# Optimization experiments

Hardware: AMD Instinct MI355X
Metric: run time of the kernel (lower is better)

The kernel has to match this reference:

```python
import jax, jax.numpy as jnp
import numpy as np

VOCAB, EMB, HID, CTXD = 32000, 512, 1024, 2048
B, T, L = 64, 64, 64

def setup_inputs() -> dict:
    key = jax.random.key(0)
    ks = jax.random.split(key, 10)
    return {
        "tgt": jax.random.randint(ks[0], (B, T), 0, VOCAB, dtype=jnp.int64 if jax.config.jax_enable_x64 else jnp.int32),
        "ctx": jax.random.normal(ks[1], (B, L, CTXD), dtype=jnp.float32),
        "h0": jax.random.normal(ks[2], (B, HID), dtype=jnp.float32),
        "ctx_lengths": jax.random.randint(ks[3], (B,), 1, L + 1),
        "emb_table": jax.random.normal(ks[4], (VOCAB, EMB), dtype=jnp.float32) * 0.01,
        "W_a": jax.random.normal(ks[5], (HID, CTXD), dtype=jnp.float32) * 0.01,
        "W_ih": jax.random.normal(ks[6], (3 * HID, EMB + CTXD), dtype=jnp.float32) * 0.01,
        "W_hh": jax.random.normal(ks[7], (3 * HID, HID), dtype=jnp.float32) * 0.01,
        "b_ih": jnp.zeros((3 * HID,), dtype=jnp.float32),
        "b_hh": jnp.zeros((3 * HID,), dtype=jnp.float32),
    }

def reference(tgt, ctx, h0, ctx_lengths, emb_table, W_a, W_ih, W_hh, b_ih, b_hh):
    H = h0.shape[-1]
    Lc = ctx.shape[1]
    # length mask over context positions: [B, L]
    mask = jnp.arange(Lc)[None, :] < ctx_lengths[:, None]
    # precompute 'general' attention projection of ctx: [B, L, H]
    ctxW = jnp.einsum('blc,hc->blh', ctx, W_a)
    emb = emb_table[tgt]  # [B, T, E]

    def step(h, e_t):
        # Bahdanau-style: attend with previous hidden state
        scores = jnp.einsum('bh,blh->bl', h, ctxW)
        scores = jnp.where(mask, scores, jnp.float32(-1e9))
        attn = jax.nn.softmax(scores, axis=-1)
        c_t = jnp.einsum('bl,blc->bc', attn, ctx)  # [B, CTXD]
        x = jnp.concatenate([e_t, c_t], axis=-1)   # [B, E+CTXD]
        gx = x @ W_ih.T + b_ih                      # [B, 3H]
        gh = h @ W_hh.T + b_hh                      # [B, 3H]
        r = jax.nn.sigmoid(gx[:, :H] + gh[:, :H])
        z = jax.nn.sigmoid(gx[:, H:2 * H] + gh[:, H:2 * H])
        n = jnp.tanh(gx[:, 2 * H:] + r * gh[:, 2 * H:])
        h_new = (1.0 - z) * n + z * h
        return h_new, h_new

    h_last, outs = jax.lax.scan(step, h0, jnp.swapaxes(emb, 0, 1))
    return jnp.swapaxes(outs, 0, 1), h_last  # (B, T, H), (B, H)
```

## Files before the change

kernel.cpp:

```cpp
#include <hip/hip_runtime.h>
#include <hip/hip_bf16.h>


using short8 = __attribute__((ext_vector_type(8))) short;
using f32x4  = __attribute__((ext_vector_type(4))) float;

#define FLAG_ACC 1
#define FLAG_BF  2

__device__ __forceinline__ void gld16(const void* g, void* l) {
  __builtin_amdgcn_global_load_lds(
      (const __attribute__((address_space(1))) unsigned int*)g,
      (__attribute__((address_space(3))) unsigned int*)l, 16, 0, 0);
}


__global__ __launch_bounds__(256) void split_bf16_kernel(
    const float* __restrict__ x, __hip_bfloat16* __restrict__ hi,
    __hip_bfloat16* __restrict__ lo, int n)
{
  int i = blockIdx.x * blockDim.x + threadIdx.x;
  int stride = gridDim.x * blockDim.x;
  for (; i < n; i += stride) {
    float v = x[i];
    __hip_bfloat16 h = __float2bfloat16(v);
    hi[i] = h;
    lo[i] = __float2bfloat16(v - __bfloat162float(h));
  }
}

__global__ __launch_bounds__(256) void prep_weights(
    const float* __restrict__ Wih, const float* __restrict__ Whh,
    const float* __restrict__ bih, const float* __restrict__ bhh,
    __hip_bfloat16* __restrict__ WcH, __hip_bfloat16* __restrict__ WcL,
    __hip_bfloat16* __restrict__ We,
    __hip_bfloat16* __restrict__ WhH, __hip_bfloat16* __restrict__ WhL,
    float* __restrict__ bihp, float* __restrict__ bhhp)
{
  const int jp = blockIdx.x;
  const int u = jp / 3, g = jp - 3 * u;
  const int src = g * 1024 + u;
  for (int c = threadIdx.x; c < 2048; c += 256) {
    float v = Wih[(size_t)src * 2560 + 512 + c];
    __hip_bfloat16 h = __float2bfloat16(v);
    WcH[(size_t)jp * 2048 + c] = h;
    WcL[(size_t)jp * 2048 + c] = __float2bfloat16(v - __bfloat162float(h));
  }
  for (int c = threadIdx.x; c < 512; c += 256)
    We[(size_t)jp * 512 + c] = __float2bfloat16(Wih[(size_t)src * 2560 + c]);
  for (int c = threadIdx.x; c < 1024; c += 256) {
    float v = Whh[(size_t)src * 1024 + c];
    __hip_bfloat16 h = __float2bfloat16(v);
    WhH[(size_t)jp * 1024 + c] = h;
    WhL[(size_t)jp * 1024 + c] = __float2bfloat16(v - __bfloat162float(h));
  }
  if (threadIdx.x == 0) { bihp[jp] = bih[src]; bhhp[jp] = bhh[src]; }
}

__global__ __launch_bounds__(256) void emb_gather(
    const int* __restrict__ tgt, const float* __restrict__ table,
    __hip_bfloat16* __restrict__ outb)
{
  const int row = blockIdx.x;
  const int v = tgt[row];
  for (int c = threadIdx.x; c < 512; c += 256)
    outb[(size_t)row * 512 + c] = __float2bfloat16(table[(size_t)v * 512 + c]);
}

__global__ __launch_bounds__(256) void h0_init(
    const float* __restrict__ h0, float* __restrict__ hf,
    __hip_bfloat16* __restrict__ hhi, __hip_bfloat16* __restrict__ hlo)
{
  const int i = blockIdx.x * 256 + threadIdx.x;
  float v = h0[i];
  hf[i] = v;
  __hip_bfloat16 h = __float2bfloat16(v);
  hhi[i] = h;
  hlo[i] = __float2bfloat16(v - __bfloat162float(h));
}


__global__ __launch_bounds__(256) void gemm_bt(
    const short* __restrict__ A, const short* __restrict__ B,
    float* __restrict__ Cf, __hip_bfloat16* __restrict__ Cb,
    const float* __restrict__ bias, int M, int N, int K, int flags)
{
  __shared__ __align__(16) short As[128 * 32];
  __shared__ __align__(16) short Bs[128 * 32];
  const int tid = threadIdx.x, lane = tid & 63, w = tid >> 6;
  const int m0 = blockIdx.y * 128, n0 = blockIdx.x * 128;
  const int wm = (w >> 1) * 64, wn = (w & 1) * 64;
  const int srow = lane >> 2;
  const int scol = (((lane & 3) ^ ((lane >> 3) & 3)) * 8);
  f32x4 zero = {0.f, 0.f, 0.f, 0.f};
  f32x4 acc[4][4];
#pragma unroll
  for (int i = 0; i < 4; ++i)
#pragma unroll
    for (int j = 0; j < 4; ++j) acc[i][j] = zero;

  for (int k0 = 0; k0 < K; k0 += 32) {
    __syncthreads();
#pragma unroll
    for (int s = 0; s < 2; ++s) {
      const int chunk = w * 2 + s;
      const int r = chunk * 16 + srow;
      gld16(A + (size_t)(m0 + r) * K + k0 + scol, As + chunk * 512);
      gld16(B + (size_t)(n0 + r) * K + k0 + scol, Bs + chunk * 512);
    }
    __syncthreads();
    const int fm = lane & 15, fq = lane >> 4;
    const int cbs = (fq ^ ((fm >> 1) & 3)) * 8;
    short8 af[4], bq[4];
#pragma unroll
    for (int i = 0; i < 4; ++i)
      af[i] = *(const short8*)(As + (wm + i * 16 + fm) * 32 + cbs);
#pragma unroll
    for (int j = 0; j < 4; ++j)
      bq[j] = *(const short8*)(Bs + (wn + j * 16 + fm) * 32 + cbs);
#pragma unroll
    for (int i = 0; i < 4; ++i)
#pragma unroll
      for (int j = 0; j < 4; ++j)
        acc[i][j] = __builtin_amdgcn_mfma_f32_16x16x32_bf16(af[i], bq[j], acc[i][j], 0, 0, 0);
  }

  const int cn = lane & 15, cq = (lane >> 4) * 4;
#pragma unroll
  for (int i = 0; i < 4; ++i)
#pragma unroll
    for (int j = 0; j < 4; ++j)
#pragma unroll
      for (int r = 0; r < 4; ++r) {
        const int m = m0 + wm + i * 16 + cq + r;
        const int n = n0 + wn + j * 16 + cn;
        float v = acc[i][j][r];
        if (flags & FLAG_ACC) v += Cf[(size_t)m * N + n];
        if (bias) v += bias[n];
        if (flags & FLAG_BF) Cb[(size_t)m * N + n] = __float2bfloat16(v);
        else                 Cf[(size_t)m * N + n] = v;
      }
}


__global__ __launch_bounds__(256) void gemm_bt3(
    const short* __restrict__ AH, const short* __restrict__ AL,
    const short* __restrict__ BH, const short* __restrict__ BL,
    float* __restrict__ Cf, int M, int N, int K)
{
  __shared__ __align__(16) short AsH[128 * 32];
  __shared__ __align__(16) short AsL[128 * 32];
  __shared__ __align__(16) short BsH[128 * 32];
  __shared__ __align__(16) short BsL[128 * 32];
  const int tid = threadIdx.x, lane = tid & 63, w = tid >> 6;
  const int m0 = blockIdx.y * 128, n0 = blockIdx.x * 128;
  const int wm = (w >> 1) * 64, wn = (w & 1) * 64;
  const int srow = lane >> 2;
  const int scol = (((lane & 3) ^ ((lane >> 3) & 3)) * 8);
  f32x4 zero = {0.f, 0.f, 0.f, 0.f};
  f32x4 acc[4][4];
#pragma unroll
  for (int i = 0; i < 4; ++i)
#pragma unroll
    for (int j = 0; j < 4; ++j) acc[i][j] = zero;

  for (int k0 = 0; k0 < K; k0 += 32) {
    __syncthreads();
#pragma unroll
    for (int s = 0; s < 2; ++s) {
      const int chunk = w * 2 + s;
      const int r = chunk * 16 + srow;
      const size_t ao = (size_t)(m0 + r) * K + k0 + scol;
      const size_t bo = (size_t)(n0 + r) * K + k0 + scol;
      gld16(AH + ao, AsH + chunk * 512);
      gld16(AL + ao, AsL + chunk * 512);
      gld16(BH + bo, BsH + chunk * 512);
      gld16(BL + bo, BsL + chunk * 512);
    }
    __syncthreads();
    const int fm = lane & 15, fq = lane >> 4;
    const int cbs = (fq ^ ((fm >> 1) & 3)) * 8;
    short8 ah[4], al[4], bh[4], bl[4];
#pragma unroll
    for (int i = 0; i < 4; ++i) {
      const int off = (wm + i * 16 + fm) * 32 + cbs;
      ah[i] = *(const short8*)(AsH + off);
      al[i] = *(const short8*)(AsL + off);
    }
#pragma unroll
    for (int j = 0; j < 4; ++j) {
      const int off = (wn + j * 16 + fm) * 32 + cbs;
      bh[j] = *(const short8*)(BsH + off);
      bl[j] = *(const short8*)(BsL + off);
    }
#pragma unroll
    for (int i = 0; i < 4; ++i)
#pragma unroll
      for (int j = 0; j < 4; ++j) {
        acc[i][j] = __builtin_amdgcn_mfma_f32_16x16x32_bf16(ah[i], bh[j], acc[i][j], 0, 0, 0);
        acc[i][j] = __builtin_amdgcn_mfma_f32_16x16x32_bf16(al[i], bh[j], acc[i][j], 0, 0, 0);
        acc[i][j] = __builtin_amdgcn_mfma_f32_16x16x32_bf16(ah[i], bl[j], acc[i][j], 0, 0, 0);
      }
  }

  const int cn = lane & 15, cq = (lane >> 4) * 4;
#pragma unroll
  for (int i = 0; i < 4; ++i)
#pragma unroll
    for (int j = 0; j < 4; ++j)
#pragma unroll
      for (int r = 0; r < 4; ++r) {
        const int m = m0 + wm + i * 16 + cq + r;
        const int n = n0 + wn + j * 16 + cn;
        Cf[(size_t)m * N + n] = acc[i][j][r];
      }
}


__global__ __launch_bounds__(256) void step_a(
    const float* __restrict__ hf, const float* __restrict__ ctxW,
    const int* __restrict__ lens, float* __restrict__ attn,
    const short* __restrict__ hhi, const short* __restrict__ hlo,
    const short* __restrict__ WhH, const short* __restrict__ WhL,
    float* __restrict__ ghG)
{
  const int tid = threadIdx.x;
  if (blockIdx.x < 64) {
    __shared__ float hs[1024];
    __shared__ float part[256];
    const int b = blockIdx.x;
    const int len = lens[b];
    ((float4*)hs)[tid] = ((const float4*)(hf + b * 1024))[tid];
    __syncthreads();
    const int l = tid >> 2, q = tid & 3;
    float sx = 0.f, sy = 0.f, sz = 0.f, sw = 0.f;
    if (l < len) {
      const float4* row = (const float4*)(ctxW + ((size_t)(b * 64 + l)) * 1024 + q * 256);
      const float4* hh = (const float4*)(hs + q * 256);
#pragma unroll 8
      for (int i = 0; i < 64; ++i) {
        float4 a = row[i], c = hh[i];
        sx += a.x * c.x; sy += a.y * c.y; sz += a.z * c.z; sw += a.w * c.w;
      }
    }
    part[tid] = (sx + sy) + (sz + sw);
    __syncthreads();
    if (tid < 64) {
      float sc = part[tid * 4] + part[tid * 4 + 1] + part[tid * 4 + 2] + part[tid * 4 + 3];
      if (tid >= len) sc = -1e9f;
      float m = sc;
#pragma unroll
      for (int off = 32; off > 0; off >>= 1) m = fmaxf(m, __shfl_xor(m, off));
      float e = __expf(sc - m);
      float sum = e;
#pragma unroll
      for (int off = 32; off > 0; off >>= 1) sum += __shfl_xor(sum, off);
      attn[b * 64 + tid] = e / sum;
    }
  } else {
    const int j0 = (blockIdx.x - 64) * 16;
    const int lane = tid & 63, w = tid >> 6;
    const int fm = lane & 15, fq = lane >> 4;
    f32x4 acc = {0.f, 0.f, 0.f, 0.f};
    const short* ah = hhi + (w * 16 + fm) * 1024 + fq * 8;
    const short* al = hlo + (w * 16 + fm) * 1024 + fq * 8;
    const short* bh = WhH + (size_t)(j0 + fm) * 1024 + fq * 8;
    const short* bl = WhL + (size_t)(j0 + fm) * 1024 + fq * 8;
#pragma unroll 4
    for (int k0 = 0; k0 < 1024; k0 += 32) {
      short8 aH = *(const short8*)(ah + k0);
      short8 aL = *(const short8*)(al + k0);
      short8 b0 = *(const short8*)(bh + k0);
      short8 c0 = *(const short8*)(bl + k0);
      acc = __builtin_amdgcn_mfma_f32_16x16x32_bf16(aH, b0, acc, 0, 0, 0);
      acc = __builtin_amdgcn_mfma_f32_16x16x32_bf16(aL, b0, acc, 0, 0, 0);
      acc = __builtin_amdgcn_mfma_f32_16x16x32_bf16(aH, c0, acc, 0, 0, 0);
    }
    const int mb = w * 16 + fq * 4;
    *(f32x4*)(ghG + (size_t)(j0 + fm) * 64 + mb) = acc;
  }
}


__global__ __launch_bounds__(512) void gate_kernel(
    const float* __restrict__ attn, const int* __restrict__ lens,
    const float* __restrict__ ghG, const float* __restrict__ ctxWc,
    const __hip_bfloat16* __restrict__ gxe, const float* __restrict__ bhhp,
    float* __restrict__ hf, short* __restrict__ hhi, short* __restrict__ hlo,
    float* __restrict__ out, int t)
{
  const int jc = blockIdx.x & 63, bc = blockIdx.x >> 6;
  const int j0 = jc * 48, b0 = bc * 8;
  __shared__ float ghs[48 * 9];
  __shared__ float wv[8][64];
  __shared__ short lidx[8][64];
  __shared__ int   cnt[8];
  __shared__ float ps0[384], ps1[384], ps2[384];
  const int tid = threadIdx.x;
  if (tid < 8) cnt[tid] = 0;
  if (tid < 384) {
    const int row = tid >> 3, col = tid & 7;
    ghs[row * 9 + col] = ghG[(size_t)(j0 + row) * 64 + b0 + col];
  }
  __syncthreads();
  if (tid < 128) {
    const int bb = tid >> 4, l4 = (tid & 15) * 4;
    const int b = b0 + bb, len = lens[b];
#pragma unroll
    for (int k = 0; k < 4; ++k) {
      const int l = l4 + k;
      const float wl = attn[b * 64 + l];
      if (l < len && wl >= 1e-8f) {
        const int pos = atomicAdd(&cnt[bb], 1);
        lidx[bb][pos] = (short)l;
        wv[bb][pos] = wl;
      }
    }
  }
  __syncthreads();

  const int q = tid >> 7, tl = tid & 127;
  const int bb = tl >> 4, jg = tl & 15;
  const int b = b0 + bb;
  const int n = cnt[bb];
  const int ibeg = (q * n) >> 2;
  const int iend = ((q + 1) * n) >> 2;
  float g0 = 0.f, g1 = 0.f, g2 = 0.f;
  const float* base = ctxWc + (size_t)(b * 64) * 3072 + j0 + jg * 3;
  int i = ibeg;
  for (; i + 3 < iend; i += 4) {
    const float w0 = wv[bb][i],     w1 = wv[bb][i + 1];
    const float w2 = wv[bb][i + 2], w3 = wv[bb][i + 3];
    const float* p0 = base + (size_t)lidx[bb][i] * 3072;
    const float* p1 = base + (size_t)lidx[bb][i + 1] * 3072;
    const float* p2 = base + (size_t)lidx[bb][i + 2] * 3072;
    const float* p3 = base + (size_t)lidx[bb][i + 3] * 3072;
    const float a0 = __builtin_nontemporal_load(p0);
    const float a1 = __builtin_nontemporal_load(p0 + 1);
    const float a2 = __builtin_nontemporal_load(p0 + 2);
    const float b0v = __builtin_nontemporal_load(p1);
    const float b1v = __builtin_nontemporal_load(p1 + 1);
    const float b2v = __builtin_nontemporal_load(p1 + 2);
    const float c0 = __builtin_nontemporal_load(p2);
    const float c1 = __builtin_nontemporal_load(p2 + 1);
    const float c2 = __builtin_nontemporal_load(p2 + 2);
    const float d0 = __builtin_nontemporal_load(p3);
    const float d1 = __builtin_nontemporal_load(p3 + 1);
    const float d2 = __builtin_nontemporal_load(p3 + 2);
    g0 += (w0 * a0 + w1 * b0v) + (w2 * c0 + w3 * d0);
    g1 += (w0 * a1 + w1 * b1v) + (w2 * c1 + w3 * d1);
    g2 += (w0 * a2 + w1 * b2v) + (w2 * c2 + w3 * d2);
  }
  for (; i < iend; ++i) {
    const float wa = wv[bb][i];
    const float* pa = base + (size_t)lidx[bb][i] * 3072;
    g0 += wa * __builtin_nontemporal_load(pa);
    g1 += wa * __builtin_nontemporal_load(pa + 1);
    g2 += wa * __builtin_nontemporal_load(pa + 2);
  }
  if (q) {
    const int o = (q - 1) * 128 + tl;
    ps0[o] = g0; ps1[o] = g1; ps2[o] = g2;
  }
  __syncthreads();
  if (q == 0) {
    g0 += (ps0[tl] + ps0[128 + tl]) + ps0[256 + tl];
    g1 += (ps1[tl] + ps1[128 + tl]) + ps1[256 + tl];
    g2 += (ps2[tl] + ps2[128 + tl]) + ps2[256 + tl];

    const int jp = j0 + jg * 3;
    const __hip_bfloat16* ge = gxe + (size_t)(b * 64 + t) * 3072 + jp;
    const float gxr = g0 + __bfloat162float(ge[0]);
    const float gxz = g1 + __bfloat162float(ge[1]);
    const float gxn = g2 + __bfloat162float(ge[2]);
    const float ghr = ghs[(jg * 3 + 0) * 9 + bb] + bhhp[jp + 0];
    const float ghz = ghs[(jg * 3 + 1) * 9 + bb] + bhhp[jp + 1];
    const float ghn = ghs[(jg * 3 + 2) * 9 + bb] + bhhp[jp + 2];
    const float rr = 1.f / (1.f + __expf(-(gxr + ghr)));
    const float zz = 1.f / (1.f + __expf(-(gxz + ghz)));
    const float nn = tanhf(gxn + rr * ghn);
    const int u = jc * 16 + jg;
    const float hold = hf[b * 1024 + u];
    const float hn = (1.f - zz) * nn + zz * hold;
    out[(size_t)(b * 64 + t) * 1024 + u] = hn;
    hf[b * 1024 + u] = hn;
    __hip_bfloat16 hh = __float2bfloat16(hn);
    hhi[b * 1024 + u] = *reinterpret_cast<short*>(&hh);
    __hip_bfloat16 hl = __float2bfloat16(hn - __bfloat162float(hh));
    hlo[b * 1024 + u] = *reinterpret_cast<short*>(&hl);
    if (t == 63) out[(size_t)64 * 64 * 1024 + b * 1024 + u] = hn;
  }
}


extern "C" void kernel_launch(void* const* d_in, const int* in_sizes, int n_in,
                              void* d_out, int out_size, void* d_ws, size_t ws_size,
                              hipStream_t stream)
{
  const int*   tgt  = (const int*)  d_in[0];
  const float* ctx  = (const float*)d_in[1];
  const float* h0   = (const float*)d_in[2];
  const int*   lens = (const int*)  d_in[3];
  const float* embt = (const float*)d_in[4];
  const float* Wa   = (const float*)d_in[5];
  const float* Wih  = (const float*)d_in[6];
  const float* Whh  = (const float*)d_in[7];
  const float* bih  = (const float*)d_in[8];
  const float* bhh  = (const float*)d_in[9];
  float* out = (float*)d_out;

  char* p = (char*)d_ws;
  auto take = [&](size_t bytes) {
    char* q = p;
    p += (bytes + 255) & ~(size_t)255;
    return q;
  };
  short* ctx_hi = (short*)take((size_t)8388608 * 2);
  short* ctx_lo = (short*)take((size_t)8388608 * 2);
  short* Wa_hi  = (short*)take((size_t)2097152 * 2);
  short* Wa_lo  = (short*)take((size_t)2097152 * 2);
  short* WcH    = (short*)take((size_t)3072 * 2048 * 2);
  short* WcL    = (short*)take((size_t)3072 * 2048 * 2);
  short* We_p   = (short*)take((size_t)3072 * 512 * 2);
  short* WhH    = (short*)take((size_t)3072 * 1024 * 2);
  short* WhL    = (short*)take((size_t)3072 * 1024 * 2);
  float* bih_p  = (float*)take(3072 * 4);
  float* bhh_p  = (float*)take(3072 * 4);
  short* emb_bf = (short*)take((size_t)4096 * 512 * 2);
  float* ctxW   = (float*)take((size_t)4096 * 1024 * 4);
  float* ctxWc  = (float*)take((size_t)4096 * 3072 * 4);
  short* gxe    = (short*)take((size_t)4096 * 3072 * 2);
  float* hf     = (float*)take((size_t)65536 * 4);
  short* hhi    = (short*)take((size_t)65536 * 2);
  short* hlo    = (short*)take((size_t)65536 * 2);
  float* attn   = (float*)take((size_t)4096 * 4);
  float* ghG    = (float*)take((size_t)3072 * 64 * 4);

  split_bf16_kernel<<<2048, 256, 0, stream>>>(ctx, (__hip_bfloat16*)ctx_hi,
                                              (__hip_bfloat16*)ctx_lo, 8388608);
  split_bf16_kernel<<<1024, 256, 0, stream>>>(Wa, (__hip_bfloat16*)Wa_hi,
                                              (__hip_bfloat16*)Wa_lo, 2097152);
  prep_weights<<<3072, 256, 0, stream>>>(Wih, Whh, bih, bhh,
      (__hip_bfloat16*)WcH, (__hip_bfloat16*)WcL, (__hip_bfloat16*)We_p,
      (__hip_bfloat16*)WhH, (__hip_bfloat16*)WhL, bih_p, bhh_p);
  emb_gather<<<4096, 256, 0, stream>>>(tgt, embt, (__hip_bfloat16*)emb_bf);
  h0_init<<<256, 256, 0, stream>>>(h0, hf, (__hip_bfloat16*)hhi,
                                   (__hip_bfloat16*)hlo);

  gemm_bt3<<<dim3(8, 32), 256, 0, stream>>>(ctx_hi, ctx_lo, Wa_hi, Wa_lo,
                                            ctxW, 4096, 1024, 2048);
  gemm_bt3<<<dim3(24, 32), 256, 0, stream>>>(ctx_hi, ctx_lo, WcH, WcL,
                                             ctxWc, 4096, 3072, 2048);
  gemm_bt<<<dim3(24, 32), 256, 0, stream>>>(emb_bf, We_p, nullptr,
                                            (__hip_bfloat16*)gxe, bih_p,
                                            4096, 3072, 512, FLAG_BF);

  for (int t = 0; t < 64; ++t) {
    step_a<<<256, 256, 0, stream>>>(hf, ctxW, lens, attn,
                                    hhi, hlo, WhH, WhL, ghG);
    gate_kernel<<<512, 512, 0, stream>>>(attn, lens, ghG, ctxWc,
        (const __hip_bfloat16*)gxe, bhh_p, hf, hhi, hlo, out, t);
  }
}
```

Before: 2.284 ms.

## Split attention scores across more blocks and move softmax into gate kernel

Attention scoring in step_a now runs on 256 blocks (four per batch row, 16 context positions each) instead of 64, and each block writes raw scores instead of normalised weights. The softmax (masking, max, exp, sum) is recomputed redundantly in gate_kernel by the otherwise idle threads 384-511, overlapping with the ghG tile load and removing one barrier. This spreads the serial per-step scoring over more CUs at the cost of redundant softmax work in every gate block and a larger launch grid.

```diff
diff --git a/kernel.cpp b/kernel.cpp
--- a/kernel.cpp
+++ b/kernel.cpp
@@ -219,46 +219,35 @@
 
 __global__ __launch_bounds__(256) void step_a(
     const float* __restrict__ hf, const float* __restrict__ ctxW,
-    const int* __restrict__ lens, float* __restrict__ attn,
+    const int* __restrict__ lens, float* __restrict__ scoresG,
     const short* __restrict__ hhi, const short* __restrict__ hlo,
     const short* __restrict__ WhH, const short* __restrict__ WhL,
     float* __restrict__ ghG)
 {
   const int tid = threadIdx.x;
-  if (blockIdx.x < 64) {
+  if (blockIdx.x < 256) {
     __shared__ float hs[1024];
-    __shared__ float part[256];
-    const int b = blockIdx.x;
+    const int b = blockIdx.x >> 2, lc = blockIdx.x & 3;
     const int len = lens[b];
     ((float4*)hs)[tid] = ((const float4*)(hf + b * 1024))[tid];
     __syncthreads();
-    const int l = tid >> 2, q = tid & 3;
-    float sx = 0.f, sy = 0.f, sz = 0.f, sw = 0.f;
+    const int l = lc * 16 + (tid >> 4), dq = tid & 15;
     if (l < len) {
-      const float4* row = (const float4*)(ctxW + ((size_t)(b * 64 + l)) * 1024 + q * 256);
-      const float4* hh = (const float4*)(hs + q * 256);
-#pragma unroll 8
-      for (int i = 0; i < 64; ++i) {
-        float4 a = row[i], c = hh[i];
+      const float4* row = (const float4*)(ctxW + (size_t)(b * 64 + l) * 1024);
+      const float4* hh = (const float4*)hs;
+      float sx = 0.f, sy = 0.f, sz = 0.f, sw = 0.f;
+#pragma unroll
+      for (int i = 0; i < 16; ++i) {
+        float4 a = row[i * 16 + dq], c = hh[i * 16 + dq];
         sx += a.x * c.x; sy += a.y * c.y; sz += a.z * c.z; sw += a.w * c.w;
       }
-    }
-    part[tid] = (sx + sy) + (sz + sw);
-    __syncthreads();
-    if (tid < 64) {
-      float sc = part[tid * 4] + part[tid * 4 + 1] + part[tid * 4 + 2] + part[tid * 4 + 3];
-      if (tid >= len) sc = -1e9f;
-      float m = sc;
-#pragma unroll
-      for (int off = 32; off > 0; off >>= 1) m = fmaxf(m, __shfl_xor(m, off));
-      float e = __expf(sc - m);
-      float sum = e;
-#pragma unroll
-      for (int off = 32; off > 0; off >>= 1) sum += __shfl_xor(sum, off);
-      attn[b * 64 + tid] = e / sum;
+      float s = (sx + sy) + (sz + sw);
+#pragma unroll
+      for (int off = 8; off > 0; off >>= 1) s += __shfl_xor(s, off);
+      if (dq == 0) scoresG[b * 64 + l] = s;
     }
   } else {
-    const int j0 = (blockIdx.x - 64) * 16;
+    const int j0 = (blockIdx.x - 256) * 16;
     const int lane = tid & 63, w = tid >> 6;
     const int fm = lane & 15, fq = lane >> 4;
     f32x4 acc = {0.f, 0.f, 0.f, 0.f};
@@ -283,7 +272,7 @@
 
 
 __global__ __launch_bounds__(512) void gate_kernel(
-    const float* __restrict__ attn, const int* __restrict__ lens,
+    const float* __restrict__ scoresG, const int* __restrict__ lens,
     const float* __restrict__ ghG, const float* __restrict__ ctxWc,
     const __hip_bfloat16* __restrict__ gxe, const float* __restrict__ bhhp,
     float* __restrict__ hf, short* __restrict__ hhi, short* __restrict__ hlo,
@@ -297,19 +286,34 @@
   __shared__ int   cnt[8];
   __shared__ float ps0[384], ps1[384], ps2[384];
   const int tid = threadIdx.x;
-  if (tid < 8) cnt[tid] = 0;
   if (tid < 384) {
     const int row = tid >> 3, col = tid & 7;
     ghs[row * 9 + col] = ghG[(size_t)(j0 + row) * 64 + b0 + col];
-  }
-  __syncthreads();
-  if (tid < 128) {
-    const int bb = tid >> 4, l4 = (tid & 15) * 4;
+  } else {
+    const int tt = tid - 384;
+    const int bb = tt >> 4, l4 = (tt & 15) * 4;
     const int b = b0 + bb, len = lens[b];
+    if ((tt & 15) == 0) cnt[bb] = 0;
+    float sc[4];
 #pragma unroll
     for (int k = 0; k < 4; ++k) {
       const int l = l4 + k;
-      const float wl = attn[b * 64 + l];
+      sc[k] = (l < len) ? scoresG[b * 64 + l] : -1e9f;
+    }
+    float m = fmaxf(fmaxf(sc[0], sc[1]), fmaxf(sc[2], sc[3]));
+#pragma unroll
+    for (int off = 8; off > 0; off >>= 1) m = fmaxf(m, __shfl_xor(m, off));
+    float e[4];
+    float s = 0.f;
+#pragma unroll
+    for (int k = 0; k < 4; ++k) { e[k] = __expf(sc[k] - m); s += e[k]; }
+#pragma unroll
+    for (int off = 8; off > 0; off >>= 1) s += __shfl_xor(s, off);
+    const float inv = 1.f / s;
+#pragma unroll
+    for (int k = 0; k < 4; ++k) {
+      const int l = l4 + k;
+      const float wl = e[k] * inv;
       if (l < len && wl >= 1e-8f) {
         const int pos = atomicAdd(&cnt[bb], 1);
         lidx[bb][pos] = (short)l;
@@ -433,7 +437,7 @@
   float* hf     = (float*)take((size_t)65536 * 4);
   short* hhi    = (short*)take((size_t)65536 * 2);
   short* hlo    = (short*)take((size_t)65536 * 2);
-  float* attn   = (float*)take((size_t)4096 * 4);
+  float* scoresG= (float*)take((size_t)4096 * 4);
   float* ghG    = (float*)take((size_t)3072 * 64 * 4);
 
   split_bf16_kernel<<<2048, 256, 0, stream>>>(ctx, (__hip_bfloat16*)ctx_hi,
@@ -456,9 +460,9 @@
                                             4096, 3072, 512, FLAG_BF);
 
   for (int t = 0; t < 64; ++t) {
-    step_a<<<256, 256, 0, stream>>>(hf, ctxW, lens, attn,
+    step_a<<<448, 256, 0, stream>>>(hf, ctxW, lens, scoresG,
                                     hhi, hlo, WhH, WhL, ghG);
-    gate_kernel<<<512, 512, 0, stream>>>(attn, lens, ghG, ctxWc,
+    gate_kernel<<<512, 512, 0, stream>>>(scoresG, lens, ghG, ctxWc,
         (const __hip_bfloat16*)gxe, bhh_p, hf, hhi, hlo, out, t);
   }
 }
```

Measured after the change: 2.337 ms. +2.3%, slower.
